# Optimization experiments

Measured on AMD Instinct MI355X. Metric: run time of the kernel, lower is better.

## Reference

```python
import jax, jax.numpy as jnp
import numpy as np

N = 100000
E = 1600000
F_IN = 1433
HID = 64
HEADS = 2
CLS = 7


def setup_inputs() -> dict:
    key = jax.random.key(0)
    ks = jax.random.split(key, 12)
    x = jax.random.normal(ks[0], (N, F_IN), dtype=jnp.float32)
    edge_index = jax.random.randint(ks[1], (2, E), 0, N, dtype=jnp.int32)
    s1 = 1.0 / np.sqrt(F_IN)
    s2 = 1.0 / np.sqrt(HID)
    W1 = jax.random.uniform(ks[2], (F_IN, HID), jnp.float32, -s1, s1)
    b1 = jnp.zeros((HID,), jnp.float32)
    W2 = jax.random.uniform(ks[3], (HID, HID), jnp.float32, -s2, s2)
    b2 = jnp.zeros((HID,), jnp.float32)
    Wg = jax.random.uniform(ks[4], (HID, HEADS * CLS), jnp.float32, -s2, s2)
    att_src = jax.random.normal(ks[5], (HEADS, CLS), jnp.float32) * 0.1
    att_dst = jax.random.normal(ks[6], (HEADS, CLS), jnp.float32) * 0.1
    bg = jnp.zeros((HEADS * CLS,), jnp.float32)
    return {"x": x, "edge_index": edge_index, "W1": W1, "b1": b1,
            "W2": W2, "b2": b2, "Wg": Wg, "att_src": att_src,
            "att_dst": att_dst, "bg": bg}


def _add_self_loops(edge_index, n):
    loop = jnp.arange(n, dtype=edge_index.dtype)
    src = jnp.concatenate([edge_index[0], loop])
    dst = jnp.concatenate([edge_index[1], loop])
    return src, dst


def _gcn_layer(x, W, b, src, dst, n):
    # symmetric normalization with self-loops (PyG GCNConv)
    deg = jax.ops.segment_sum(jnp.ones_like(src, dtype=x.dtype), dst, num_segments=n)
    dinv = jnp.where(deg > 0, jax.lax.rsqrt(deg), 0.0)
    norm = dinv[src] * dinv[dst]  # [E+N]
    h = x @ W  # transform before propagate (in >= out)
    msg = h[src] * norm[:, None]
    out = jax.ops.segment_sum(msg, dst, num_segments=n)
    return out + b


def _gat_layer(x, Wg, att_src, att_dst, bg, src, dst, n):
    h = (x @ Wg).reshape(n, HEADS, CLS)  # [N,H,C]
    a_src = jnp.sum(h * att_src, axis=-1)  # [N,H]
    a_dst = jnp.sum(h * att_dst, axis=-1)
    e = jax.nn.leaky_relu(a_src[src] + a_dst[dst], 0.2)  # [E+N,H]
    m = jax.ops.segment_max(e, dst, num_segments=n)  # [N,H]
    m = jnp.where(jnp.isfinite(m), m, 0.0)
    p = jnp.exp(e - m[dst])
    s = jax.ops.segment_sum(p, dst, num_segments=n)
    alpha = p / (s[dst] + 1e-16)  # segment softmax, [E+N,H]
    out = jax.ops.segment_sum(h[src] * alpha[:, :, None], dst, num_segments=n)
    return out.reshape(n, HEADS * CLS) + bg


def reference(x, edge_index, W1, b1, W2, b2, Wg, att_src, att_dst, bg):
    src, dst = _add_self_loops(edge_index, N)
    h = jax.nn.relu(_gcn_layer(x, W1, b1, src, dst, N))
    h = jax.nn.relu(_gcn_layer(h, W2, b2, src, dst, N))
    h = _gat_layer(h, Wg, att_src, att_dst, bg, src, dst, N)
    return jax.nn.log_softmax(h, axis=1)
```

## Files before the change

kernel.cpp:

```cpp
#include <hip/hip_runtime.h>
#include <hip/hip_bf16.h>

#define F_IN 1433
#define HID  64
#define C14  14

typedef __attribute__((ext_vector_type(8))) short short8;
typedef __attribute__((ext_vector_type(4))) float float4v;

__device__ inline short f2bf(float f) {
    union { float f; unsigned u; } c; c.f = f;
    unsigned u = c.u;
    u += 0x7fffu + ((u >> 16) & 1u);
    return (short)(u >> 16);
}

__device__ inline unsigned packbf(float a, float b) {
    union { float f; unsigned u; } x, y;
    x.f = a; y.f = b;
    unsigned ua = x.u; ua += 0x7fffu + ((ua >> 16) & 1u);
    unsigned ub = y.u; ub += 0x7fffu + ((ub >> 16) & 1u);
    return (ua >> 16) | (ub & 0xffff0000u);
}

__device__ inline float bflo(unsigned u) {
    union { unsigned u; float f; } c; c.u = u << 16; return c.f;
}
__device__ inline float bfhi(unsigned u) {
    union { unsigned u; float f; } c; c.u = u & 0xffff0000u; return c.f;
}


__global__ void k_setup(const float* __restrict__ W1, const float* __restrict__ W2,
                        short* __restrict__ Bf1, short* __restrict__ Bf2,
                        int* __restrict__ cnt, int n, int prep1, int prep2) {
    int i = blockIdx.x * 256 + threadIdx.x;
    if (i < prep1 + prep2) {
        const float* W; short* Bf; int K; int id;
        if (i < prep1) { W = W1; Bf = Bf1; K = F_IN; id = i; }
        else           { W = W2; Bf = Bf2; K = 64;   id = i - prep1; }
        int l = id & 63;
        int s = (id >> 6) & 1;
        int t = (id >> 7) & 3;
        int ks = id >> 9;
        int nn = t * 16 + (l & 15);
        int k0 = ks * 64 + s * 32 + (l >> 4) * 8;
        short tmp[8];
#pragma unroll
        for (int j = 0; j < 8; j++) {
            int k = k0 + j;
            tmp[j] = (k < K) ? f2bf(W[(size_t)k * 64 + nn]) : (short)0;
        }
        *(short8*)&Bf[(size_t)id * 8] = *(const short8*)tmp;
    }
    if (i < n) cnt[i] = 0;
}


__global__ void k_hist(const int* __restrict__ dst, int* __restrict__ cnt, int E) {
    int e = blockIdx.x * 256 + threadIdx.x;
    if (e < E) atomicAdd(&cnt[dst[e]], 1);
}

__global__ __launch_bounds__(1024) void k_scan1(const int* __restrict__ cnt,
                                                int* __restrict__ excl,
                                                int* __restrict__ bsum,
                                                float* __restrict__ dinv, int n) {
    __shared__ int sd[1024];
    int tid = threadIdx.x;
    int g = blockIdx.x * 1024 + tid;
    int v = (g < n) ? cnt[g] : 0;
    if (g < n) dinv[g] = rsqrtf((float)v + 1.0f);
    sd[tid] = v;
    __syncthreads();
    for (int off = 1; off < 1024; off <<= 1) {
        int t = (tid >= off) ? sd[tid - off] : 0;
        __syncthreads();
        sd[tid] += t;
        __syncthreads();
    }
    if (g < n) excl[g] = sd[tid] - v;
    if (tid == 1023) bsum[blockIdx.x] = sd[1023];
}

__global__ __launch_bounds__(128) void k_scan2(const int* __restrict__ bsum,
                                               int* __restrict__ boff, int nb) {
    __shared__ int sd[128];
    int tid = threadIdx.x;
    int v = (tid < nb) ? bsum[tid] : 0;
    sd[tid] = v;
    __syncthreads();
    for (int off = 1; off < 128; off <<= 1) {
        int t = (tid >= off) ? sd[tid - off] : 0;
        __syncthreads();
        sd[tid] += t;
        __syncthreads();
    }
    if (tid < nb) boff[tid] = sd[tid] - v;
}

__global__ __launch_bounds__(1024) void k_scan3(int* __restrict__ rowst,
                                                const int* __restrict__ boff,
                                                int* __restrict__ fill, int n, int E) {
    int tid = threadIdx.x;
    int g = blockIdx.x * 1024 + tid;
    if (g < n) {
        int v = rowst[g] + boff[blockIdx.x];
        rowst[g] = v;
        fill[g] = v;
    }
    if (g == 0) rowst[n] = E;
}

__global__ void k_scatter(const int* __restrict__ ei, int* __restrict__ fill,
                          int* __restrict__ esrc, int E) {
    int e = blockIdx.x * 256 + threadIdx.x;
    if (e < E) {
        int s = ei[e];
        int d = ei[E + e];
        int pos = atomicAdd(&fill[d], 1);
        esrc[pos] = s;
    }
}


__global__ __launch_bounds__(256) void gemm_mfma(const float* __restrict__ A, int K, int nchunk,
                                                 int M, const short* __restrict__ Bf,
                                                 const float* __restrict__ dinv,
                                                 unsigned* __restrict__ C) {
    __shared__ short As[128 * 64];
    __shared__ short Bs[4096];
    const int tid = threadIdx.x;
    const int w = tid >> 6, l = tid & 63;
    const int row0 = blockIdx.x * 128;
    const int m16 = l & 15, q = l >> 4;

    const int lrow = tid >> 5;
    const int lcol = (tid & 31) * 2;
    const bool interior = (row0 + 128 <= M);
    const size_t rs = (size_t)K;
    const float* __restrict__ Abase = A + (size_t)min(row0 + lrow, M - 1) * rs + lcol;

    float4v acc[2][4];
#pragma unroll
    for (int mi = 0; mi < 2; mi++)
#pragma unroll
        for (int t = 0; t < 4; t++) acc[mi][t] = (float4v){0.f, 0.f, 0.f, 0.f};

    float pre[32];
    int4 preB0, preB1;

    auto issue = [&](int ks) {
        const int kb = ks * 64;
        if (interior && (kb + 64 <= K)) {
#pragma unroll
            for (int it = 0; it < 16; it++) {
                const float* p2 = Abase + kb + (size_t)(it * 8) * rs;
                pre[2 * it]     = p2[0];
                pre[2 * it + 1] = p2[1];
            }
        } else {
#pragma unroll
            for (int it = 0; it < 16; it++) {
                int row = min(row0 + it * 8 + lrow, M - 1);
                int c = kb + lcol;
                const float* p2 = A + (size_t)row * rs + c;
                pre[2 * it]     = (c < K)     ? p2[0] : 0.f;
                pre[2 * it + 1] = (c + 1 < K) ? p2[1] : 0.f;
            }
        }
        const short* bsrc = Bf + (size_t)ks * 4096;
        preB0 = *(const int4*)&bsrc[tid * 16];
        preB1 = *(const int4*)&bsrc[tid * 16 + 8];
    };

    auto stage = [&]() {
        char* As8 = (char*)As;
#pragma unroll
        for (int it = 0; it < 16; it++) {
            int row = it * 8 + lrow;
            unsigned u = packbf(pre[2 * it], pre[2 * it + 1]);
            int p = lcol >> 3;
            int pp = p ^ (row & 7);
            *(unsigned*)&As8[row * 128 + pp * 16 + (lcol & 7) * 2] = u;
        }
        *(int4*)&Bs[tid * 16] = preB0;
        *(int4*)&Bs[tid * 16 + 8] = preB1;
    };

    auto compute = [&]() {
#pragma unroll
        for (int s = 0; s < 2; s++) {
            short8 a[2];
#pragma unroll
            for (int mi = 0; mi < 2; mi++) {
                int row = w * 32 + mi * 16 + m16;
                int p = s * 4 + q;
                a[mi] = *(const short8*)&As[row * 64 + (p ^ (row & 7)) * 8];
            }
#pragma unroll
            for (int t = 0; t < 4; t++) {
                short8 b = *(const short8*)&Bs[(t * 2 + s) * 512 + l * 8];
                acc[0][t] = __builtin_amdgcn_mfma_f32_16x16x32_bf16(a[0], b, acc[0][t], 0, 0, 0);
                acc[1][t] = __builtin_amdgcn_mfma_f32_16x16x32_bf16(a[1], b, acc[1][t], 0, 0, 0);
            }
        }
    };

    issue(0);
    stage();
    __syncthreads();
    for (int ks = 0; ks < nchunk; ks++) {
        bool more = (ks + 1 < nchunk);
        if (more) issue(ks + 1);
        compute();
        __syncthreads();
        if (more) {
            stage();
            __syncthreads();
        }
    }

#pragma unroll
    for (int mi = 0; mi < 2; mi++) {
#pragma unroll
        for (int i = 0; i < 4; i++) {
            int rr = row0 + w * 32 + mi * 16 + q * 4 + i;
            if (rr < M) {
                float dv = dinv ? dinv[rr] : 1.f;
                uint2 uu;
                uu.x = packbf(acc[0 + mi * 0][0][0], 0.f);
                uu.x = packbf(acc[mi][0][i] * dv, acc[mi][1][i] * dv);
                uu.y = packbf(acc[mi][2][i] * dv, acc[mi][3][i] * dv);
                *(uint2*)&C[(size_t)rr * 32 + 2 * m16] = uu;
            }
        }
    }
}


__global__ __launch_bounds__(256) void gcn_prop(const uint2* __restrict__ Hb, float* __restrict__ O,
                                                const int* __restrict__ rowst,
                                                const int* __restrict__ esrc,
                                                const float* __restrict__ dinv,
                                                const float* __restrict__ bias, int n) {
    int i = blockIdx.x * 16 + (threadIdx.x >> 4);
    if (i >= n) return;
    int L = threadIdx.x & 15;
    const uint2* __restrict__ Hr = Hb + L;

    uint2 sv = Hr[(size_t)i * 16];
    float a0 = bflo(sv.x), a1 = bfhi(sv.x), a2 = bflo(sv.y), a3 = bfhi(sv.y);

    int j0 = rowst[i], j1 = rowst[i + 1];
    int j = j0;
    for (; j + 8 <= j1; j += 8) {
        int s[8];
#pragma unroll
        for (int u = 0; u < 8; u++) s[u] = esrc[j + u];
        uint2 v[8];
#pragma unroll
        for (int u = 0; u < 8; u++) v[u] = Hr[(size_t)s[u] * 16];
        float t0 = ((bflo(v[0].x) + bflo(v[1].x)) + (bflo(v[2].x) + bflo(v[3].x)))
                 + ((bflo(v[4].x) + bflo(v[5].x)) + (bflo(v[6].x) + bflo(v[7].x)));
        float t1 = ((bfhi(v[0].x) + bfhi(v[1].x)) + (bfhi(v[2].x) + bfhi(v[3].x)))
                 + ((bfhi(v[4].x) + bfhi(v[5].x)) + (bfhi(v[6].x) + bfhi(v[7].x)));
        float t2 = ((bflo(v[0].y) + bflo(v[1].y)) + (bflo(v[2].y) + bflo(v[3].y)))
                 + ((bflo(v[4].y) + bflo(v[5].y)) + (bflo(v[6].y) + bflo(v[7].y)));
        float t3 = ((bfhi(v[0].y) + bfhi(v[1].y)) + (bfhi(v[2].y) + bfhi(v[3].y)))
                 + ((bfhi(v[4].y) + bfhi(v[5].y)) + (bfhi(v[6].y) + bfhi(v[7].y)));
        a0 += t0; a1 += t1; a2 += t2; a3 += t3;
    }
    if (j + 4 <= j1) {
        int s[4];
#pragma unroll
        for (int u = 0; u < 4; u++) s[u] = esrc[j + u];
        uint2 v[4];
#pragma unroll
        for (int u = 0; u < 4; u++) v[u] = Hr[(size_t)s[u] * 16];
        a0 += (bflo(v[0].x) + bflo(v[1].x)) + (bflo(v[2].x) + bflo(v[3].x));
        a1 += (bfhi(v[0].x) + bfhi(v[1].x)) + (bfhi(v[2].x) + bfhi(v[3].x));
        a2 += (bflo(v[0].y) + bflo(v[1].y)) + (bflo(v[2].y) + bflo(v[3].y));
        a3 += (bfhi(v[0].y) + bfhi(v[1].y)) + (bfhi(v[2].y) + bfhi(v[3].y));
        j += 4;
    }
    for (; j < j1; j++) {
        uint2 v = Hr[(size_t)esrc[j] * 16];
        a0 += bflo(v.x); a1 += bfhi(v.x); a2 += bflo(v.y); a3 += bfhi(v.y);
    }

    float di = dinv[i];
    float o0 = fmaxf(a0 * di + bias[L],      0.f);
    float o1 = fmaxf(a1 * di + bias[L + 16], 0.f);
    float o2 = fmaxf(a2 * di + bias[L + 32], 0.f);
    float o3 = fmaxf(a3 * di + bias[L + 48], 0.f);
    float* Or = O + (size_t)i * 64;
    Or[L] = o0; Or[L + 16] = o1; Or[L + 32] = o2; Or[L + 48] = o3;
}


__global__ __launch_bounds__(256) void gat_gemm(const float* __restrict__ X,
                                                const float* __restrict__ Wg,
                                                const float* __restrict__ att_src,
                                                const float* __restrict__ att_dst,
                                                float* __restrict__ HG,
                                                float* __restrict__ AD,
                                                int n) {
    __shared__ float xs[64 * 65];
    __shared__ float wg[64 * C14];
    __shared__ float hgs[64 * 15];
    const int tid = threadIdx.x;
    const int n0 = blockIdx.x * 64;

    for (int i = tid; i < 64 * C14; i += 256) wg[i] = Wg[i];
    for (int i = tid * 4; i < 4096; i += 1024) {
        int nn = i >> 6, k = i & 63;
        int g = n0 + nn;
        float4 v = make_float4(0.f, 0.f, 0.f, 0.f);
        if (g < n) v = *(const float4*)&X[(size_t)g * 64 + k];
        xs[nn * 65 + k] = v.x;
        xs[nn * 65 + k + 1] = v.y;
        xs[nn * 65 + k + 2] = v.z;
        xs[nn * 65 + k + 3] = v.w;
    }
    __syncthreads();

    const int nn = tid & 63;
    const int qq = tid >> 6;
    float acc[4] = {0.f, 0.f, 0.f, 0.f};
    for (int k = 0; k < 64; k++) {
        float a = xs[nn * 65 + k];
#pragma unroll
        for (int j = 0; j < 4; j++) {
            int c = qq + 4 * j;
            if (c < C14) acc[j] += a * wg[k * C14 + c];
        }
    }
    int g = n0 + nn;
#pragma unroll
    for (int j = 0; j < 4; j++) {
        int c = qq + 4 * j;
        if (c < C14) {
            hgs[nn * 15 + c] = acc[j];
            if (g < n) HG[(size_t)g * 16 + c] = acc[j];
        }
    }
    __syncthreads();

    if (tid < 128) {
        int nloc = tid & 63;
        int h = tid >> 6;
        int gg = n0 + nloc;
        if (gg < n) {
            float s1 = 0.f, s2 = 0.f;
#pragma unroll
            for (int cc = 0; cc < 7; cc++) {
                float hv = hgs[nloc * 15 + h * 7 + cc];
                s1 += hv * att_src[h * 7 + cc];
                s2 += hv * att_dst[h * 7 + cc];
            }
            HG[(size_t)gg * 16 + 14 + h] = s1;
            AD[(size_t)gg * 2 + h] = s2;
        }
    }
}


__global__ __launch_bounds__(256) void gat_agg(const float* __restrict__ HG,
                                               const float* __restrict__ AD,
                                               const int* __restrict__ rowst,
                                               const int* __restrict__ esrc,
                                               const float* __restrict__ bg,
                                               float* __restrict__ out, int n) {
    int i = blockIdx.x * 16 + (threadIdx.x >> 4);
    if (i >= n) return;
    int c = threadIdx.x & 15;
    int h = (c < 7) ? 0 : 1;
    int asl = 14 + h;
    float adst = AD[(size_t)i * 2 + h];
    auto lrelu = [](float x) { return x > 0.f ? x : 0.2f * x; };

    float gself = HG[(size_t)i * 16 + c];
    float asrc = __shfl(gself, asl, 16);
    float m = lrelu(asrc + adst);
    float ssum = 1.f;
    float acc = (c < C14) ? gself : 0.f;

    int j0 = rowst[i], j1 = rowst[i + 1];
    int j = j0;
    for (; j + 8 <= j1; j += 8) {
        int s[8];
#pragma unroll
        for (int u = 0; u < 8; u++) s[u] = esrc[j + u];
        float gv[8], e[8];
#pragma unroll
        for (int u = 0; u < 8; u++) gv[u] = HG[(size_t)s[u] * 16 + c];
#pragma unroll
        for (int u = 0; u < 8; u++) {
            e[u] = lrelu(__shfl(gv[u], asl, 16) + adst);
            if (c >= C14) gv[u] = 0.f;
        }
        float em = fmaxf(fmaxf(fmaxf(e[0], e[1]), fmaxf(e[2], e[3])),
                         fmaxf(fmaxf(e[4], e[5]), fmaxf(e[6], e[7])));
        float nm = fmaxf(m, em);
        float sc = __expf(m - nm);
        float p[8];
#pragma unroll
        for (int u = 0; u < 8; u++) p[u] = __expf(e[u] - nm);
        float ps = ((p[0] + p[1]) + (p[2] + p[3])) + ((p[4] + p[5]) + (p[6] + p[7]));
        float gs = ((gv[0] * p[0] + gv[1] * p[1]) + (gv[2] * p[2] + gv[3] * p[3]))
                 + ((gv[4] * p[4] + gv[5] * p[5]) + (gv[6] * p[6] + gv[7] * p[7]));
        ssum = ssum * sc + ps;
        acc = acc * sc + gs;
        m = nm;
    }
    if (j + 4 <= j1) {
        int s[4];
#pragma unroll
        for (int u = 0; u < 4; u++) s[u] = esrc[j + u];
        float gv[4], e[4];
#pragma unroll
        for (int u = 0; u < 4; u++) gv[u] = HG[(size_t)s[u] * 16 + c];
#pragma unroll
        for (int u = 0; u < 4; u++) {
            e[u] = lrelu(__shfl(gv[u], asl, 16) + adst);
            if (c >= C14) gv[u] = 0.f;
        }
        float em = fmaxf(fmaxf(e[0], e[1]), fmaxf(e[2], e[3]));
        float nm = fmaxf(m, em);
        float sc = __expf(m - nm);
        float p[4];
#pragma unroll
        for (int u = 0; u < 4; u++) p[u] = __expf(e[u] - nm);
        float ps = (p[0] + p[1]) + (p[2] + p[3]);
        float gs = (gv[0] * p[0] + gv[1] * p[1]) + (gv[2] * p[2] + gv[3] * p[3]);
        ssum = ssum * sc + ps;
        acc = acc * sc + gs;
        m = nm;
        j += 4;
    }
    for (; j < j1; j++) {
        float gv = HG[(size_t)esrc[j] * 16 + c];
        float e = lrelu(__shfl(gv, asl, 16) + adst);
        if (c >= C14) gv = 0.f;
        float nm = fmaxf(m, e);
        float sc = __expf(m - nm);
        float pe = __expf(e - nm);
        ssum = ssum * sc + pe;
        acc = acc * sc + gv * pe;
        m = nm;
    }

    float v = acc / ssum + ((c < C14) ? bg[c] : 0.f);

    float vv = (c < C14) ? v : -__builtin_inff();
    float maxv = vv;
#pragma unroll
    for (int d = 1; d < 16; d <<= 1) maxv = fmaxf(maxv, __shfl_xor(maxv, d, 16));
    float ee = (c < C14) ? __expf(v - maxv) : 0.f;
    float s2 = ee;
#pragma unroll
    for (int d = 1; d < 16; d <<= 1) s2 += __shfl_xor(s2, d, 16);
    if (c < C14) out[(size_t)i * C14 + c] = v - maxv - __logf(s2);
}


extern "C" void kernel_launch(void* const* d_in, const int* in_sizes, int n_in,
                              void* d_out, int out_size, void* d_ws, size_t ws_size,
                              hipStream_t stream) {
    const float* x       = (const float*)d_in[0];
    const int*   ei      = (const int*)d_in[1];
    const float* W1      = (const float*)d_in[2];
    const float* b1      = (const float*)d_in[3];
    const float* W2      = (const float*)d_in[4];
    const float* b2      = (const float*)d_in[5];
    const float* Wg      = (const float*)d_in[6];
    const float* att_src = (const float*)d_in[7];
    const float* att_dst = (const float*)d_in[8];
    const float* bg      = (const float*)d_in[9];

    const int N = in_sizes[0] / F_IN;
    const int E = in_sizes[1] / 2;
    const int NC1 = (F_IN + 63) / 64;
    const int NC2 = 1;

    char* p = (char*)d_ws;
    auto alloc = [&](size_t bytes) {
        char* r = p;
        p += (bytes + 255) & ~(size_t)255;
        return r;
    };
    unsigned* h = (unsigned*)alloc((size_t)N * 32 * 4);
    float* g    = (float*)alloc((size_t)N * 64 * 4);
    float* hg   = (float*)alloc((size_t)N * 16 * 4);
    float* Ad   = (float*)alloc((size_t)N * 2 * 4);
    float* dinv = (float*)alloc((size_t)N * 4);
    int* cnt    = (int*)alloc((size_t)N * 4);
    int* rowst  = (int*)alloc((size_t)(N + 1) * 4);
    int* fill   = (int*)alloc((size_t)N * 4);
    int* esrc   = (int*)alloc((size_t)E * 4);
    int* bsum   = (int*)alloc(128 * 4);
    int* boff   = (int*)alloc(128 * 4);
    short* Bf1  = (short*)alloc((size_t)NC1 * 4096 * 2);
    short* Bf2  = (short*)alloc((size_t)NC2 * 4096 * 2);

    const int gN = (N + 255) / 256;
    const int gE = (E + 255) / 256;
    const int nb = (N + 1023) / 1024;
    const int g16 = (N + 15) / 16;
    const int gT64 = (N + 63) / 64;
    const int gT128 = (N + 127) / 128;
    const int prep1 = NC1 * 512, prep2 = NC2 * 512;

    k_setup<<<gN, 256, 0, stream>>>(W1, W2, Bf1, Bf2, cnt, N, prep1, prep2);

    k_hist<<<gE, 256, 0, stream>>>(ei + E, cnt, E);
    k_scan1<<<nb, 1024, 0, stream>>>(cnt, rowst, bsum, dinv, N);
    k_scan2<<<1, 128, 0, stream>>>(bsum, boff, nb);
    k_scan3<<<nb, 1024, 0, stream>>>(rowst, boff, fill, N, E);
    k_scatter<<<gE, 256, 0, stream>>>(ei, fill, esrc, E);

    gemm_mfma<<<gT128, 256, 0, stream>>>(x, F_IN, NC1, N, Bf1, dinv, h);
    gcn_prop<<<g16, 256, 0, stream>>>((const uint2*)h, g, rowst, esrc, dinv, b1, N);
    gemm_mfma<<<gT128, 256, 0, stream>>>(g, 64, NC2, N, Bf2, dinv, h);
    gcn_prop<<<g16, 256, 0, stream>>>((const uint2*)h, g, rowst, esrc, dinv, b2, N);
    gat_gemm<<<gT64, 256, 0, stream>>>(g, Wg, att_src, att_dst, hg, Ad, N);
    gat_agg<<<g16, 256, 0, stream>>>(hg, Ad, rowst, esrc, bg, (float*)d_out, N);
}
```

Measured before the change: 1.145 ms.

## Fuse GCN propagation with following GEMMs to avoid fp32 intermediates

```diff
diff --git a/kernel.cpp b/kernel.cpp
--- a/kernel.cpp
+++ b/kernel.cpp
@@ -227,9 +227,8 @@
         for (int i = 0; i < 4; i++) {
             int rr = row0 + w * 32 + mi * 16 + q * 4 + i;
             if (rr < M) {
-                float dv = dinv ? dinv[rr] : 1.f;
+                float dv = dinv[rr];
                 uint2 uu;
-                uu.x = packbf(acc[0 + mi * 0][0][0], 0.f);
                 uu.x = packbf(acc[mi][0][i] * dv, acc[mi][1][i] * dv);
                 uu.y = packbf(acc[mi][2][i] * dv, acc[mi][3][i] * dv);
                 *(uint2*)&C[(size_t)rr * 32 + 2 * m16] = uu;
@@ -239,130 +238,232 @@
 }
 
 
-__global__ __launch_bounds__(256) void gcn_prop(const uint2* __restrict__ Hb, float* __restrict__ O,
+__global__ __launch_bounds__(256) void prop_gemm2(const uint2* __restrict__ Hb,
+                                                  const short* __restrict__ Bf,
+                                                  const int* __restrict__ rowst,
+                                                  const int* __restrict__ esrc,
+                                                  const float* __restrict__ dinv,
+                                                  const float* __restrict__ bias,
+                                                  int n, unsigned* __restrict__ C) {
+    __shared__ short As[128 * 64];
+    __shared__ short Bs[4096];
+    const int tid = threadIdx.x;
+    const int w = tid >> 6, l = tid & 63;
+    const int row0 = blockIdx.x * 128;
+    const int m16 = l & 15, q = l >> 4;
+    const int L = tid & 15;
+    const int grp = tid >> 4;
+
+    *(int4*)&Bs[tid * 16] = *(const int4*)&Bf[tid * 16];
+    *(int4*)&Bs[tid * 16 + 8] = *(const int4*)&Bf[tid * 16 + 8];
+
+    const float bb0 = bias[L], bb1 = bias[L + 16], bb2 = bias[L + 32], bb3 = bias[L + 48];
+    const uint2* __restrict__ Hr = Hb + L;
+    char* As8 = (char*)As;
+
+    for (int b = 0; b < 8; b++) {
+        const int row = b * 16 + grp;
+        const int i = row0 + row;
+        float a0 = 0.f, a1 = 0.f, a2 = 0.f, a3 = 0.f;
+        if (i < n) {
+            uint2 sv = Hr[(size_t)i * 16];
+            a0 = bflo(sv.x); a1 = bfhi(sv.x); a2 = bflo(sv.y); a3 = bfhi(sv.y);
+            int j0 = rowst[i], j1 = rowst[i + 1];
+            int j = j0;
+            for (; j + 8 <= j1; j += 8) {
+                int s[8];
+#pragma unroll
+                for (int u = 0; u < 8; u++) s[u] = esrc[j + u];
+                uint2 v[8];
+#pragma unroll
+                for (int u = 0; u < 8; u++) v[u] = Hr[(size_t)s[u] * 16];
+                a0 += ((bflo(v[0].x) + bflo(v[1].x)) + (bflo(v[2].x) + bflo(v[3].x)))
+                    + ((bflo(v[4].x) + bflo(v[5].x)) + (bflo(v[6].x) + bflo(v[7].x)));
+                a1 += ((bfhi(v[0].x) + bfhi(v[1].x)) + (bfhi(v[2].x) + bfhi(v[3].x)))
+                    + ((bfhi(v[4].x) + bfhi(v[5].x)) + (bfhi(v[6].x) + bfhi(v[7].x)));
+                a2 += ((bflo(v[0].y) + bflo(v[1].y)) + (bflo(v[2].y) + bflo(v[3].y)))
+                    + ((bflo(v[4].y) + bflo(v[5].y)) + (bflo(v[6].y) + bflo(v[7].y)));
+                a3 += ((bfhi(v[0].y) + bfhi(v[1].y)) + (bfhi(v[2].y) + bfhi(v[3].y)))
+                    + ((bfhi(v[4].y) + bfhi(v[5].y)) + (bfhi(v[6].y) + bfhi(v[7].y)));
+            }
+            if (j + 4 <= j1) {
+                int s[4];
+#pragma unroll
+                for (int u = 0; u < 4; u++) s[u] = esrc[j + u];
+                uint2 v[4];
+#pragma unroll
+                for (int u = 0; u < 4; u++) v[u] = Hr[(size_t)s[u] * 16];
+                a0 += (bflo(v[0].x) + bflo(v[1].x)) + (bflo(v[2].x) + bflo(v[3].x));
+                a1 += (bfhi(v[0].x) + bfhi(v[1].x)) + (bfhi(v[2].x) + bfhi(v[3].x));
+                a2 += (bflo(v[0].y) + bflo(v[1].y)) + (bflo(v[2].y) + bflo(v[3].y));
+                a3 += (bfhi(v[0].y) + bfhi(v[1].y)) + (bfhi(v[2].y) + bfhi(v[3].y));
+                j += 4;
+            }
+            for (; j < j1; j++) {
+                uint2 v = Hr[(size_t)esrc[j] * 16];
+                a0 += bflo(v.x); a1 += bfhi(v.x); a2 += bflo(v.y); a3 += bfhi(v.y);
+            }
+            float di = dinv[i];
+            a0 = fmaxf(a0 * di + bb0, 0.f);
+            a1 = fmaxf(a1 * di + bb1, 0.f);
+            a2 = fmaxf(a2 * di + bb2, 0.f);
+            a3 = fmaxf(a3 * di + bb3, 0.f);
+        }
+        float n0 = __shfl_xor(a0, 1);
+        float n1 = __shfl_xor(a1, 1);
+        float n2 = __shfl_xor(a2, 1);
+        float n3 = __shfl_xor(a3, 1);
+        if ((L & 1) == 0) {
+            const int r7 = row & 7;
+            unsigned u0 = packbf(a0, n0);
+            unsigned u1 = packbf(a1, n1);
+            unsigned u2 = packbf(a2, n2);
+            unsigned u3 = packbf(a3, n3);
+            int ke;
+            ke = L;      *(unsigned*)&As8[row * 128 + (((ke >> 3) ^ r7) << 4) + (ke & 7) * 2] = u0;
+            ke = L + 16; *(unsigned*)&As8[row * 128 + (((ke >> 3) ^ r7) << 4) + (ke & 7) * 2] = u1;
+            ke = L + 32; *(unsigned*)&As8[row * 128 + (((ke >> 3) ^ r7) << 4) + (ke & 7) * 2] = u2;
+            ke = L + 48; *(unsigned*)&As8[row * 128 + (((ke >> 3) ^ r7) << 4) + (ke & 7) * 2] = u3;
+        }
+    }
+    __syncthreads();
+
+    float4v acc[2][4];
+#pragma unroll
+    for (int mi = 0; mi < 2; mi++)
+#pragma unroll
+        for (int t = 0; t < 4; t++) acc[mi][t] = (float4v){0.f, 0.f, 0.f, 0.f};
+
+#pragma unroll
+    for (int s = 0; s < 2; s++) {
+        short8 a[2];
+#pragma unroll
+        for (int mi = 0; mi < 2; mi++) {
+            int row = w * 32 + mi * 16 + m16;
+            int p = s * 4 + q;
+            a[mi] = *(const short8*)&As[row * 64 + (p ^ (row & 7)) * 8];
+        }
+#pragma unroll
+        for (int t = 0; t < 4; t++) {
+            short8 b = *(const short8*)&Bs[(t * 2 + s) * 512 + l * 8];
+            acc[0][t] = __builtin_amdgcn_mfma_f32_16x16x32_bf16(a[0], b, acc[0][t], 0, 0, 0);
+            acc[1][t] = __builtin_amdgcn_mfma_f32_16x16x32_bf16(a[1], b, acc[1][t], 0, 0, 0);
+        }
+    }
+
+#pragma unroll
+    for (int mi = 0; mi < 2; mi++) {
+#pragma unroll
+        for (int i = 0; i < 4; i++) {
+            int rr = row0 + w * 32 + mi * 16 + q * 4 + i;
+            if (rr < n) {
+                float dv = dinv[rr];
+                uint2 uu;
+                uu.x = packbf(acc[mi][0][i] * dv, acc[mi][1][i] * dv);
+                uu.y = packbf(acc[mi][2][i] * dv, acc[mi][3][i] * dv);
+                *(uint2*)&C[(size_t)rr * 32 + 2 * m16] = uu;
+            }
+        }
+    }
+}
+
+
+__global__ __launch_bounds__(256) void prop_gat(const uint2* __restrict__ Hb,
+                                                const float* __restrict__ Wg,
+                                                const float* __restrict__ att_src,
+                                                const float* __restrict__ att_dst,
                                                 const int* __restrict__ rowst,
                                                 const int* __restrict__ esrc,
                                                 const float* __restrict__ dinv,
-                                                const float* __restrict__ bias, int n) {
-    int i = blockIdx.x * 16 + (threadIdx.x >> 4);
-    if (i >= n) return;
-    int L = threadIdx.x & 15;
+                                                const float* __restrict__ bias,
+                                                float* __restrict__ HG, float* __restrict__ AD,
+                                                int n) {
+    __shared__ float wgs[64 * C14];
+    __shared__ float asd[28];
+    __shared__ float hs[16][65];
+    __shared__ float pr[16][34];
+    const int tid = threadIdx.x;
+    for (int i = tid; i < 64 * C14; i += 256) wgs[i] = Wg[i];
+    if (tid < 14) asd[tid] = att_src[tid];
+    else if (tid < 28) asd[tid] = att_dst[tid - 14];
+    __syncthreads();
+
+    const int L = tid & 15;
+    const int grp = tid >> 4;
+    const int i = blockIdx.x * 16 + grp;
+    const float bb0 = bias[L], bb1 = bias[L + 16], bb2 = bias[L + 32], bb3 = bias[L + 48];
     const uint2* __restrict__ Hr = Hb + L;
 
-    uint2 sv = Hr[(size_t)i * 16];
-    float a0 = bflo(sv.x), a1 = bfhi(sv.x), a2 = bflo(sv.y), a3 = bfhi(sv.y);
-
-    int j0 = rowst[i], j1 = rowst[i + 1];
-    int j = j0;
-    for (; j + 8 <= j1; j += 8) {
-        int s[8];
-#pragma unroll
-        for (int u = 0; u < 8; u++) s[u] = esrc[j + u];
-        uint2 v[8];
-#pragma unroll
-        for (int u = 0; u < 8; u++) v[u] = Hr[(size_t)s[u] * 16];
-        float t0 = ((bflo(v[0].x) + bflo(v[1].x)) + (bflo(v[2].x) + bflo(v[3].x)))
-                 + ((bflo(v[4].x) + bflo(v[5].x)) + (bflo(v[6].x) + bflo(v[7].x)));
-        float t1 = ((bfhi(v[0].x) + bfhi(v[1].x)) + (bfhi(v[2].x) + bfhi(v[3].x)))
-                 + ((bfhi(v[4].x) + bfhi(v[5].x)) + (bfhi(v[6].x) + bfhi(v[7].x)));
-        float t2 = ((bflo(v[0].y) + bflo(v[1].y)) + (bflo(v[2].y) + bflo(v[3].y)))
-                 + ((bflo(v[4].y) + bflo(v[5].y)) + (bflo(v[6].y) + bflo(v[7].y)));
-        float t3 = ((bfhi(v[0].y) + bfhi(v[1].y)) + (bfhi(v[2].y) + bfhi(v[3].y)))
-                 + ((bfhi(v[4].y) + bfhi(v[5].y)) + (bfhi(v[6].y) + bfhi(v[7].y)));
-        a0 += t0; a1 += t1; a2 += t2; a3 += t3;
-    }
-    if (j + 4 <= j1) {
-        int s[4];
-#pragma unroll
-        for (int u = 0; u < 4; u++) s[u] = esrc[j + u];
-        uint2 v[4];
-#pragma unroll
-        for (int u = 0; u < 4; u++) v[u] = Hr[(size_t)s[u] * 16];
-        a0 += (bflo(v[0].x) + bflo(v[1].x)) + (bflo(v[2].x) + bflo(v[3].x));
-        a1 += (bfhi(v[0].x) + bfhi(v[1].x)) + (bfhi(v[2].x) + bfhi(v[3].x));
-        a2 += (bflo(v[0].y) + bflo(v[1].y)) + (bflo(v[2].y) + bflo(v[3].y));
-        a3 += (bfhi(v[0].y) + bfhi(v[1].y)) + (bfhi(v[2].y) + bfhi(v[3].y));
-        j += 4;
-    }
-    for (; j < j1; j++) {
-        uint2 v = Hr[(size_t)esrc[j] * 16];
-        a0 += bflo(v.x); a1 += bfhi(v.x); a2 += bflo(v.y); a3 += bfhi(v.y);
-    }
-
-    float di = dinv[i];
-    float o0 = fmaxf(a0 * di + bias[L],      0.f);
-    float o1 = fmaxf(a1 * di + bias[L + 16], 0.f);
-    float o2 = fmaxf(a2 * di + bias[L + 32], 0.f);
-    float o3 = fmaxf(a3 * di + bias[L + 48], 0.f);
-    float* Or = O + (size_t)i * 64;
-    Or[L] = o0; Or[L + 16] = o1; Or[L + 32] = o2; Or[L + 48] = o3;
-}
-
-
-__global__ __launch_bounds__(256) void gat_gemm(const float* __restrict__ X,
-                                                const float* __restrict__ Wg,
-                                                const float* __restrict__ att_src,
-                                                const float* __restrict__ att_dst,
-                                                float* __restrict__ HG,
-                                                float* __restrict__ AD,
-                                                int n) {
-    __shared__ float xs[64 * 65];
-    __shared__ float wg[64 * C14];
-    __shared__ float hgs[64 * 15];
-    const int tid = threadIdx.x;
-    const int n0 = blockIdx.x * 64;
-
-    for (int i = tid; i < 64 * C14; i += 256) wg[i] = Wg[i];
-    for (int i = tid * 4; i < 4096; i += 1024) {
-        int nn = i >> 6, k = i & 63;
-        int g = n0 + nn;
-        float4 v = make_float4(0.f, 0.f, 0.f, 0.f);
-        if (g < n) v = *(const float4*)&X[(size_t)g * 64 + k];
-        xs[nn * 65 + k] = v.x;
-        xs[nn * 65 + k + 1] = v.y;
-        xs[nn * 65 + k + 2] = v.z;
-        xs[nn * 65 + k + 3] = v.w;
-    }
+    float a0 = 0.f, a1 = 0.f, a2 = 0.f, a3 = 0.f;
+    if (i < n) {
+        uint2 sv = Hr[(size_t)i * 16];
+        a0 = bflo(sv.x); a1 = bfhi(sv.x); a2 = bflo(sv.y); a3 = bfhi(sv.y);
+        int j0 = rowst[i], j1 = rowst[i + 1];
+        int j = j0;
+        for (; j + 8 <= j1; j += 8) {
+            int s[8];
+#pragma unroll
+            for (int u = 0; u < 8; u++) s[u] = esrc[j + u];
+            uint2 v[8];
+#pragma unroll
+            for (int u = 0; u < 8; u++) v[u] = Hr[(size_t)s[u] * 16];
+            a0 += ((bflo(v[0].x) + bflo(v[1].x)) + (bflo(v[2].x) + bflo(v[3].x)))
+                + ((bflo(v[4].x) + bflo(v[5].x)) + (bflo(v[6].x) + bflo(v[7].x)));
+            a1 += ((bfhi(v[0].x) + bfhi(v[1].x)) + (bfhi(v[2].x) + bfhi(v[3].x)))
+                + ((bfhi(v[4].x) + bfhi(v[5].x)) + (bfhi(v[6].x) + bfhi(v[7].x)));
+            a2 += ((bflo(v[0].y) + bflo(v[1].y)) + (bflo(v[2].y) + bflo(v[3].y)))
+                + ((bflo(v[4].y) + bflo(v[5].y)) + (bflo(v[6].y) + bflo(v[7].y)));
+            a3 += ((bfhi(v[0].y) + bfhi(v[1].y)) + (bfhi(v[2].y) + bfhi(v[3].y)))
+                + ((bfhi(v[4].y) + bfhi(v[5].y)) + (bfhi(v[6].y) + bfhi(v[7].y)));
+        }
+        if (j + 4 <= j1) {
+            int s[4];
+#pragma unroll
+            for (int u = 0; u < 4; u++) s[u] = esrc[j + u];
+            uint2 v[4];
+#pragma unroll
+            for (int u = 0; u < 4; u++) v[u] = Hr[(size_t)s[u] * 16];
+            a0 += (bflo(v[0].x) + bflo(v[1].x)) + (bflo(v[2].x) + bflo(v[3].x));
+            a1 += (bfhi(v[0].x) + bfhi(v[1].x)) + (bfhi(v[2].x) + bfhi(v[3].x));
+            a2 += (bflo(v[0].y) + bflo(v[1].y)) + (bflo(v[2].y) + bflo(v[3].y));
+            a3 += (bfhi(v[0].y) + bfhi(v[1].y)) + (bfhi(v[2].y) + bfhi(v[3].y));
+            j += 4;
+        }
+        for (; j < j1; j++) {
+            uint2 v = Hr[(size_t)esrc[j] * 16];
+            a0 += bflo(v.x); a1 += bfhi(v.x); a2 += bflo(v.y); a3 += bfhi(v.y);
+        }
+        float di = dinv[i];
+        a0 = fmaxf(a0 * di + bb0, 0.f);
+        a1 = fmaxf(a1 * di + bb1, 0.f);
+        a2 = fmaxf(a2 * di + bb2, 0.f);
+        a3 = fmaxf(a3 * di + bb3, 0.f);
+    }
+    hs[grp][L] = a0; hs[grp][L + 16] = a1; hs[grp][L + 32] = a2; hs[grp][L + 48] = a3;
     __syncthreads();
 
-    const int nn = tid & 63;
-    const int qq = tid >> 6;
-    float acc[4] = {0.f, 0.f, 0.f, 0.f};
-    for (int k = 0; k < 64; k++) {
-        float a = xs[nn * 65 + k];
-#pragma unroll
-        for (int j = 0; j < 4; j++) {
-            int c = qq + 4 * j;
-            if (c < C14) acc[j] += a * wg[k * C14 + c];
-        }
-    }
-    int g = n0 + nn;
-#pragma unroll
-    for (int j = 0; j < 4; j++) {
-        int c = qq + 4 * j;
-        if (c < C14) {
-            hgs[nn * 15 + c] = acc[j];
-            if (g < n) HG[(size_t)g * 16 + c] = acc[j];
-        }
-    }
+    float hg = 0.f;
+    if (L < C14) {
+        const float* hrow = hs[grp];
+        for (int k = 0; k < 64; k++) hg += hrow[k] * wgs[k * C14 + L];
+    }
+    pr[grp][L]      = (L < C14) ? hg * asd[L]      : 0.f;
+    pr[grp][17 + L] = (L < C14) ? hg * asd[14 + L] : 0.f;
     __syncthreads();
 
-    if (tid < 128) {
-        int nloc = tid & 63;
-        int h = tid >> 6;
-        int gg = n0 + nloc;
-        if (gg < n) {
-            float s1 = 0.f, s2 = 0.f;
-#pragma unroll
-            for (int cc = 0; cc < 7; cc++) {
-                float hv = hgs[nloc * 15 + h * 7 + cc];
-                s1 += hv * att_src[h * 7 + cc];
-                s2 += hv * att_dst[h * 7 + cc];
-            }
-            HG[(size_t)gg * 16 + 14 + h] = s1;
-            AD[(size_t)gg * 2 + h] = s2;
-        }
-    }
+    float outv = hg;
+    if (L >= C14) {
+        int hh = L - 14;
+        float s1 = 0.f, s2 = 0.f;
+#pragma unroll
+        for (int cc = 0; cc < 7; cc++) {
+            s1 += pr[grp][hh * 7 + cc];
+            s2 += pr[grp][17 + hh * 7 + cc];
+        }
+        outv = s1;
+        if (i < n) AD[(size_t)i * 2 + hh] = s2;
+    }
+    if (i < n) HG[(size_t)i * 16 + L] = outv;
 }
 
 
@@ -490,8 +591,8 @@
         p += (bytes + 255) & ~(size_t)255;
         return r;
     };
-    unsigned* h = (unsigned*)alloc((size_t)N * 32 * 4);
-    float* g    = (float*)alloc((size_t)N * 64 * 4);
+    unsigned* h  = (unsigned*)alloc((size_t)N * 32 * 4);
+    unsigned* h2 = (unsigned*)alloc((size_t)N * 32 * 4);
     float* hg   = (float*)alloc((size_t)N * 16 * 4);
     float* Ad   = (float*)alloc((size_t)N * 2 * 4);
     float* dinv = (float*)alloc((size_t)N * 4);
@@ -508,7 +609,6 @@
     const int gE = (E + 255) / 256;
     const int nb = (N + 1023) / 1024;
     const int g16 = (N + 15) / 16;
-    const int gT64 = (N + 63) / 64;
     const int gT128 = (N + 127) / 128;
     const int prep1 = NC1 * 512, prep2 = NC2 * 512;
 
@@ -521,9 +621,8 @@
     k_scatter<<<gE, 256, 0, stream>>>(ei, fill, esrc, E);
 
     gemm_mfma<<<gT128, 256, 0, stream>>>(x, F_IN, NC1, N, Bf1, dinv, h);
-    gcn_prop<<<g16, 256, 0, stream>>>((const uint2*)h, g, rowst, esrc, dinv, b1, N);
-    gemm_mfma<<<gT128, 256, 0, stream>>>(g, 64, NC2, N, Bf2, dinv, h);
-    gcn_prop<<<g16, 256, 0, stream>>>((const uint2*)h, g, rowst, esrc, dinv, b2, N);
-    gat_gemm<<<gT64, 256, 0, stream>>>(g, Wg, att_src, att_dst, hg, Ad, N);
+    prop_gemm2<<<gT128, 256, 0, stream>>>((const uint2*)h, Bf2, rowst, esrc, dinv, b1, N, h2);
+    prop_gat<<<g16, 256, 0, stream>>>((const uint2*)h2, Wg, att_src, att_dst,
+                                      rowst, esrc, dinv, b2, hg, Ad, N);
     gat_agg<<<g16, 256, 0, stream>>>(hg, Ad, rowst, esrc, bg, (float*)d_out, N);
 }
```

Measured after the change: 1.109 ms. 3.1% less time.
